# Kernel optimization log

Hardware: AMD Instinct MI355X
Metric: run time of the kernel (lower is better)

Reference implementation:

```python
import jax, jax.numpy as jnp
import numpy as np

B, C, H, W = 8, 256, 64, 64
NUM_HEADS = 4


def setup_inputs() -> dict:
    key = jax.random.key(0)
    ks = jax.random.split(key, 6)
    s = 0.02  # small init scale for 1x1 conv weights
    return {
        "x": jax.random.normal(ks[0], (B, C, H, W), jnp.float32),
        "cproj": jax.random.normal(ks[1], (B, C, H, W), jnp.float32),
        "wq": jax.random.normal(ks[2], (C, C), jnp.float32) * s,
        "bq": jnp.zeros((C,), jnp.float32),
        "wkv": jax.random.normal(ks[3], (2 * C, C), jnp.float32) * s,
        "bkv": jnp.zeros((2 * C,), jnp.float32),
        "wo": jax.random.normal(ks[4], (C, C), jnp.float32) * s,  # zero_module in torch; random here for a meaningful baseline
        "bo": jnp.zeros((C,), jnp.float32),
    }


def reference(x, cproj, wq, bq, wkv, bkv, wo, bo):
    Bb, Cc, Hh, Ww = x.shape
    N = Hh * Ww
    h = NUM_HEADS
    d = Cc // h
    scale = 1.0 / jnp.sqrt(jnp.sqrt(jnp.asarray(Cc, jnp.float32)))

    xf = x.reshape(Bb, Cc, N)
    cf = cproj.reshape(Bb, Cc, N)

    # 1x1 convs == channel matmuls
    Q = jnp.einsum('oc,bcn->bon', wq, xf) + bq[None, :, None]           # (B,C,N)
    KV = jnp.einsum('oc,bcn->bon', wkv, cf) + bkv[None, :, None]        # (B,2C,N)
    K, V = KV[:, :Cc], KV[:, Cc:]

    # softmax over channel-dim-within-head for q, over spatial N for k
    q = jax.nn.softmax(Q.reshape(Bb, h, d, N) * scale, axis=2).reshape(Bb, Cc, N)
    k = jax.nn.softmax(K.reshape(Bb, h, d, N), axis=3).reshape(Bb, Cc, N)

    # linear-attention: (B,C,C) context, then project back to N — note heads are mixed, per original bmm
    context = jnp.einsum('bcn,bdn->bcd', k, V)
    out = jnp.einsum('bcd,bdn->bcn', context, q)

    out = jnp.einsum('oc,bcn->bon', wo, out) + bo[None, :, None]
    return out.reshape(Bb, Cc, Hh, Ww)
```

## Files before the change

### kernel.cpp

```cpp
#include <hip/hip_runtime.h>

#define B_ 8
#define C_ 256
#define N_ 4096
#define NSPLIT 8

typedef float f32x4 __attribute__((ext_vector_type(4)));
typedef __bf16 bf16x8 __attribute__((ext_vector_type(8)));
typedef unsigned short u16x8 __attribute__((ext_vector_type(8)));
typedef unsigned short u16x4 __attribute__((ext_vector_type(4)));

__device__ __forceinline__ unsigned short f2bf(float f) {
  unsigned u = __float_as_uint(f);
  u += 0x7fff + ((u >> 16) & 1);
  return (unsigned short)(u >> 16);
}

__device__ __forceinline__ f32x4 mfma16(bf16x8 a, bf16x8 b, f32x4 c) {
  return __builtin_amdgcn_mfma_f32_16x16x32_bf16(a, b, c, 0, 0, 0);
}

typedef __attribute__((address_space(1))) const void* gvp;
typedef __attribute__((address_space(3))) void* lvp;
__device__ __forceinline__ void gld16(const void* g, void* l) {
  __builtin_amdgcn_global_load_lds((gvp)g, (lvp)l, 16, 0, 0);
}

template <int ROWS>
__device__ __forceinline__ void stage(unsigned short* lds, const unsigned short* g,
                                      int ld, int w, int lane) {
  const int r8 = lane >> 3;
  const int ce = ((lane & 7) ^ r8) << 3;
  const unsigned short* gp = g + (size_t)(w * (ROWS / 4) + r8) * ld + ce;
  unsigned short* lp = lds + w * (ROWS / 4) * 64;
#pragma unroll
  for (int i = 0; i < ROWS / 32; i++)
    gld16(gp + (size_t)(i * 8) * ld, lp + i * 512);
}

__device__ __forceinline__ bf16x8 frag(const unsigned short* lds, int row, int kc) {
  return *(const bf16x8*)(lds + row * 64 + ((kc ^ (row & 7)) << 3));
}

__global__ __launch_bounds__(256) void castw(
    const float* __restrict__ wq, const float* __restrict__ wkv,
    const float* __restrict__ wo, unsigned short* __restrict__ wqb,
    unsigned short* __restrict__ wkvb, unsigned short* __restrict__ wob) {
  int i = (blockIdx.x * 256 + threadIdx.x) * 4;
  const float* src;
  unsigned short* dst;
  int off;
  if (i < 65536) { src = wq; dst = wqb; off = i; }
  else if (i < 196608) { src = wkv; dst = wkvb; off = i - 65536; }
  else { src = wo; dst = wob; off = i - 196608; }
  float4 v = *(const float4*)(src + off);
  *(u16x4*)(dst + off) = (u16x4){f2bf(v.x), f2bf(v.y), f2bf(v.z), f2bf(v.w)};
}

__global__ __launch_bounds__(256) void transpose_cast(
    const float* __restrict__ x, const float* __restrict__ cp,
    unsigned short* __restrict__ xT, unsigned short* __restrict__ cpT) {
  __shared__ unsigned short tr[64][72];
  const int z = blockIdx.z, b = z >> 1;
  const float* src = (z & 1) ? cp : x;
  unsigned short* dst = (z & 1) ? cpT : xT;
  const int c0 = blockIdx.y * 64, n0 = blockIdx.x * 64;
  const int t = threadIdx.x;
  const int row = t >> 2, cg = (t & 3) * 16;
  const float* sp = src + ((size_t)b * C_ + c0 + row) * N_ + n0 + cg;
#pragma unroll
  for (int j = 0; j < 16; j += 4) {
    float4 v = *(const float4*)(sp + j);
    tr[cg + j + 0][row] = f2bf(v.x);
    tr[cg + j + 1][row] = f2bf(v.y);
    tr[cg + j + 2][row] = f2bf(v.z);
    tr[cg + j + 3][row] = f2bf(v.w);
  }
  __syncthreads();
  unsigned short* dp = dst + ((size_t)b * N_ + n0 + row) * C_ + c0 + cg;
  *(u16x8*)dp = *(const u16x8*)&tr[row][cg];
  *(u16x8*)(dp + 8) = *(const u16x8*)&tr[row][cg + 8];
}

__global__ __launch_bounds__(256) void qproj(
    const unsigned short* __restrict__ wqb, const unsigned short* __restrict__ xT,
    const float* __restrict__ bq, unsigned short* __restrict__ qT) {
  __shared__ __align__(16) unsigned short As[128 * 64];
  __shared__ __align__(16) unsigned short Bs[128 * 64];
  const int b = blockIdx.z, m0 = blockIdx.y * 128, n0 = blockIdx.x * 128;
  const int tid = threadIdx.x, lane = tid & 63, w = tid >> 6;
  const int m0w = (w >> 1) * 64, n0w = (w & 1) * 64;
  const int colL = lane & 15, kq = lane >> 4, quad = lane >> 4;
  const unsigned short* Ag = wqb + (size_t)m0 * C_;
  const unsigned short* Bg = xT + ((size_t)b * N_ + n0) * C_;

  f32x4 acc[4][4];
#pragma unroll
  for (int i = 0; i < 4; i++)
#pragma unroll
    for (int j = 0; j < 4; j++) acc[i][j] = (f32x4){0.f, 0.f, 0.f, 0.f};

  for (int kt = 0; kt < 4; kt++) {
    stage<128>(As, Ag + kt * 64, C_, w, lane);
    stage<128>(Bs, Bg + kt * 64, C_, w, lane);
    __syncthreads();
#pragma unroll
    for (int ks = 0; ks < 2; ks++) {
      bf16x8 af[4], bf[4];
#pragma unroll
      for (int mt = 0; mt < 4; mt++) af[mt] = frag(As, m0w + mt * 16 + colL, ks * 4 + kq);
#pragma unroll
      for (int nt = 0; nt < 4; nt++) bf[nt] = frag(Bs, n0w + nt * 16 + colL, ks * 4 + kq);
#pragma unroll
      for (int mt = 0; mt < 4; mt++)
#pragma unroll
        for (int nt = 0; nt < 4; nt++) acc[mt][nt] = mfma16(af[mt], bf[nt], acc[mt][nt]);
    }
    __syncthreads();
  }

#pragma unroll
  for (int nt = 0; nt < 4; nt++) {
    float v[16];
    float mx = -1e30f;
#pragma unroll
    for (int mt = 0; mt < 4; mt++)
#pragma unroll
      for (int r = 0; r < 4; r++) {
        int m = m0 + m0w + mt * 16 + quad * 4 + r;
        float val = (acc[mt][nt][r] + bq[m]) * 0.25f;
        v[mt * 4 + r] = val;
        mx = fmaxf(mx, val);
      }
    mx = fmaxf(mx, __shfl_xor(mx, 16));
    mx = fmaxf(mx, __shfl_xor(mx, 32));
    float s = 0.f;
#pragma unroll
    for (int j = 0; j < 16; j++) { v[j] = __expf(v[j] - mx); s += v[j]; }
    s += __shfl_xor(s, 16);
    s += __shfl_xor(s, 32);
    float inv = 1.0f / s;
    const int n = n0 + n0w + nt * 16 + colL;
    unsigned short* qb = qT + ((size_t)b * N_ + n) * C_ + m0 + m0w;
#pragma unroll
    for (int mt = 0; mt < 4; mt++) {
      u16x4 o = (u16x4){f2bf(v[mt * 4 + 0] * inv), f2bf(v[mt * 4 + 1] * inv),
                        f2bf(v[mt * 4 + 2] * inv), f2bf(v[mt * 4 + 3] * inv)};
      *(u16x4*)(qb + mt * 16 + quad * 4) = o;
    }
  }
}

__global__ __launch_bounds__(256) void kvproj(
    const unsigned short* __restrict__ wkvb, const unsigned short* __restrict__ cpT,
    const float* __restrict__ bkv, float* __restrict__ Kf,
    unsigned short* __restrict__ Vb) {
  __shared__ __align__(16) unsigned short As[128 * 64];
  __shared__ __align__(16) unsigned short Bs[128 * 64];
  const int b = blockIdx.z, m0 = blockIdx.y * 128, n0 = blockIdx.x * 128;
  const int tid = threadIdx.x, lane = tid & 63, w = tid >> 6;
  const int m0w = (w >> 1) * 64, n0w = (w & 1) * 64;
  const int colL = lane & 15, kq = lane >> 4, quad = lane >> 4;
  const unsigned short* Ag = wkvb + (size_t)m0 * C_;
  const unsigned short* Bg = cpT + ((size_t)b * N_ + n0) * C_;

  f32x4 acc[4][4];
#pragma unroll
  for (int i = 0; i < 4; i++)
#pragma unroll
    for (int j = 0; j < 4; j++) acc[i][j] = (f32x4){0.f, 0.f, 0.f, 0.f};

  for (int kt = 0; kt < 4; kt++) {
    stage<128>(As, Ag + kt * 64, C_, w, lane);
    stage<128>(Bs, Bg + kt * 64, C_, w, lane);
    __syncthreads();
#pragma unroll
    for (int ks = 0; ks < 2; ks++) {
      bf16x8 af[4], bf[4];
#pragma unroll
      for (int mt = 0; mt < 4; mt++) af[mt] = frag(As, m0w + mt * 16 + colL, ks * 4 + kq);
#pragma unroll
      for (int nt = 0; nt < 4; nt++) bf[nt] = frag(Bs, n0w + nt * 16 + colL, ks * 4 + kq);
#pragma unroll
      for (int mt = 0; mt < 4; mt++)
#pragma unroll
        for (int nt = 0; nt < 4; nt++) acc[mt][nt] = mfma16(af[mt], bf[nt], acc[mt][nt]);
    }
    __syncthreads();
  }

#pragma unroll
  for (int mt = 0; mt < 4; mt++)
#pragma unroll
    for (int r = 0; r < 4; r++) {
      int m = m0 + m0w + mt * 16 + quad * 4 + r;
      float bias = bkv[m];
      if (m < C_) {
        float* kr = Kf + ((size_t)b * C_ + m) * N_ + n0 + n0w;
#pragma unroll
        for (int nt = 0; nt < 4; nt++) kr[nt * 16 + colL] = acc[mt][nt][r] + bias;
      } else {
        unsigned short* vr = Vb + ((size_t)b * C_ + m - C_) * N_ + n0 + n0w;
#pragma unroll
        for (int nt = 0; nt < 4; nt++) vr[nt * 16 + colL] = f2bf(acc[mt][nt][r] + bias);
      }
    }
}

__global__ __launch_bounds__(256) void ksoftmax(const float* __restrict__ Kf,
                                                unsigned short* __restrict__ kb) {
  const int b = blockIdx.x >> 8, c = blockIdx.x & 255;
  const float* row = Kf + ((size_t)b * C_ + c) * N_;
  unsigned short* orow = kb + ((size_t)b * C_ + c) * N_;
  const int t = threadIdx.x, lane = t & 63, wv = t >> 6;
  __shared__ float red[8];

  float4 v[4];
  float mx = -1e30f;
#pragma unroll
  for (int i = 0; i < 4; i++) {
    v[i] = *(const float4*)&row[i * 1024 + t * 4];
    mx = fmaxf(fmaxf(fmaxf(mx, v[i].x), fmaxf(v[i].y, v[i].z)), v[i].w);
  }
#pragma unroll
  for (int o = 32; o > 0; o >>= 1) mx = fmaxf(mx, __shfl_down(mx, o));
  if (lane == 0) red[wv] = mx;
  __syncthreads();
  mx = fmaxf(fmaxf(red[0], red[1]), fmaxf(red[2], red[3]));

  float s = 0.f;
#pragma unroll
  for (int i = 0; i < 4; i++) {
    v[i].x = __expf(v[i].x - mx); v[i].y = __expf(v[i].y - mx);
    v[i].z = __expf(v[i].z - mx); v[i].w = __expf(v[i].w - mx);
    s += v[i].x + v[i].y + v[i].z + v[i].w;
  }
#pragma unroll
  for (int o = 32; o > 0; o >>= 1) s += __shfl_down(s, o);
  if (lane == 0) red[4 + wv] = s;
  __syncthreads();
  float inv = 1.0f / (red[4] + red[5] + red[6] + red[7]);
#pragma unroll
  for (int i = 0; i < 4; i++) {
    u16x4 o = (u16x4){f2bf(v[i].x * inv), f2bf(v[i].y * inv),
                      f2bf(v[i].z * inv), f2bf(v[i].w * inv)};
    *(u16x4*)&orow[i * 1024 + t * 4] = o;
  }
}

__global__ __launch_bounds__(256) void ctx_part(
    const unsigned short* __restrict__ kb, const unsigned short* __restrict__ Vb,
    float* __restrict__ ctxp) {
  __shared__ __align__(16) unsigned short As[128 * 64];
  __shared__ __align__(16) unsigned short Bs[64 * 64];
  const int z = blockIdx.z, b = z >> 3, s = z & 7;
  const int m0 = blockIdx.y * 128, n0 = blockIdx.x * 64;
  const int tid = threadIdx.x, lane = tid & 63, w = tid >> 6;
  const int m0w = (w & 1) * 64, n0w = (w >> 1) * 32;
  const int colL = lane & 15, kq = lane >> 4, quad = lane >> 4;
  const unsigned short* Ag = kb + ((size_t)b * C_ + m0) * N_;
  const unsigned short* Bg = Vb + ((size_t)b * C_ + n0) * N_;
  const int kbeg = s * (N_ / NSPLIT);

  f32x4 acc[4][2];
#pragma unroll
  for (int i = 0; i < 4; i++)
#pragma unroll
    for (int j = 0; j < 2; j++) acc[i][j] = (f32x4){0.f, 0.f, 0.f, 0.f};

  for (int kt = 0; kt < (N_ / NSPLIT) / 64; kt++) {
    stage<128>(As, Ag + kbeg + kt * 64, N_, w, lane);
    stage<64>(Bs, Bg + kbeg + kt * 64, N_, w, lane);
    __syncthreads();
#pragma unroll
    for (int ks = 0; ks < 2; ks++) {
      bf16x8 af[4], bf[2];
#pragma unroll
      for (int mt = 0; mt < 4; mt++) af[mt] = frag(As, m0w + mt * 16 + colL, ks * 4 + kq);
#pragma unroll
      for (int nt = 0; nt < 2; nt++) bf[nt] = frag(Bs, n0w + nt * 16 + colL, ks * 4 + kq);
#pragma unroll
      for (int mt = 0; mt < 4; mt++)
#pragma unroll
        for (int nt = 0; nt < 2; nt++) acc[mt][nt] = mfma16(af[mt], bf[nt], acc[mt][nt]);
    }
    __syncthreads();
  }

  float* outp = ctxp + ((size_t)s * B_ + b) * C_ * C_;
#pragma unroll
  for (int mt = 0; mt < 4; mt++)
#pragma unroll
    for (int nt = 0; nt < 2; nt++)
#pragma unroll
      for (int r = 0; r < 4; r++) {
        int m = m0 + m0w + mt * 16 + quad * 4 + r;
        int n = n0 + n0w + nt * 16 + colL;
        outp[(size_t)m * C_ + n] = acc[mt][nt][r];
      }
}

__global__ __launch_bounds__(256) void ctx_reduce_t(const float* __restrict__ ctxp,
                                                    unsigned short* __restrict__ ctxsT) {
  __shared__ unsigned short t[64][72];
  const int b = blockIdx.z, c0 = blockIdx.y * 64, d0 = blockIdx.x * 64;
  const int tid = threadIdx.x;
  const int cl = tid >> 2, dg = (tid & 3) * 16;
  const float* base = ctxp + ((size_t)b * C_ + c0 + cl) * C_ + d0 + dg;
  float acc[16];
#pragma unroll
  for (int j = 0; j < 16; j++) acc[j] = 0.f;
  for (int s = 0; s < NSPLIT; s++) {
    const float* p = base + (size_t)s * B_ * C_ * C_;
#pragma unroll
    for (int j = 0; j < 16; j += 4) {
      float4 v = *(const float4*)(p + j);
      acc[j] += v.x; acc[j + 1] += v.y; acc[j + 2] += v.z; acc[j + 3] += v.w;
    }
  }
#pragma unroll
  for (int j = 0; j < 16; j++) t[dg + j][cl] = f2bf(acc[j]);
  __syncthreads();
  const int dr = tid >> 2, cg = (tid & 3) * 16;
  unsigned short* dp = ctxsT + ((size_t)b * C_ + d0 + dr) * C_ + c0 + cg;
  *(u16x8*)dp = *(const u16x8*)&t[dr][cg];
  *(u16x8*)(dp + 8) = *(const u16x8*)&t[dr][cg + 8];
}

__global__ __launch_bounds__(256) void oproj(
    const unsigned short* __restrict__ wob, const unsigned short* __restrict__ ctxsT,
    unsigned short* __restrict__ ctx2) {
  __shared__ __align__(16) unsigned short As[128 * 64];
  __shared__ __align__(16) unsigned short Bs[128 * 64];
  const int b = blockIdx.z, m0 = blockIdx.y * 128, n0 = blockIdx.x * 128;
  const int tid = threadIdx.x, lane = tid & 63, w = tid >> 6;
  const int m0w = (w >> 1) * 64, n0w = (w & 1) * 64;
  const int colL = lane & 15, kq = lane >> 4, quad = lane >> 4;
  const unsigned short* Ag = wob + (size_t)m0 * C_;
  const unsigned short* Bg = ctxsT + ((size_t)b * C_ + n0) * C_;

  f32x4 acc[4][4];
#pragma unroll
  for (int i = 0; i < 4; i++)
#pragma unroll
    for (int j = 0; j < 4; j++) acc[i][j] = (f32x4){0.f, 0.f, 0.f, 0.f};

  for (int kt = 0; kt < 4; kt++) {
    stage<128>(As, Ag + kt * 64, C_, w, lane);
    stage<128>(Bs, Bg + kt * 64, C_, w, lane);
    __syncthreads();
#pragma unroll
    for (int ks = 0; ks < 2; ks++) {
      bf16x8 af[4], bf[4];
#pragma unroll
      for (int mt = 0; mt < 4; mt++) af[mt] = frag(As, m0w + mt * 16 + colL, ks * 4 + kq);
#pragma unroll
      for (int nt = 0; nt < 4; nt++) bf[nt] = frag(Bs, n0w + nt * 16 + colL, ks * 4 + kq);
#pragma unroll
      for (int mt = 0; mt < 4; mt++)
#pragma unroll
        for (int nt = 0; nt < 4; nt++) acc[mt][nt] = mfma16(af[mt], bf[nt], acc[mt][nt]);
    }
    __syncthreads();
  }

  unsigned short* ob = ctx2 + (size_t)b * C_ * C_;
#pragma unroll
  for (int mt = 0; mt < 4; mt++)
#pragma unroll
    for (int nt = 0; nt < 4; nt++)
#pragma unroll
      for (int r = 0; r < 4; r++) {
        int m = m0 + m0w + mt * 16 + quad * 4 + r;
        int n = n0 + n0w + nt * 16 + colL;
        ob[(size_t)m * C_ + n] = f2bf(acc[mt][nt][r]);
      }
}

__global__ __launch_bounds__(256) void outgemm(
    const unsigned short* __restrict__ ctx2, const unsigned short* __restrict__ qT,
    const float* __restrict__ bo, float* __restrict__ out) {
  __shared__ __align__(16) unsigned short As[128 * 64];
  __shared__ __align__(16) unsigned short Bs[128 * 64];
  const int b = blockIdx.z, n0 = blockIdx.x * 128, m0 = blockIdx.y * 128;
  const int tid = threadIdx.x, lane = tid & 63, w = tid >> 6;
  const int m0w = (w >> 1) * 64, n0w = (w & 1) * 64;
  const int colL = lane & 15, kq = lane >> 4, quad = lane >> 4;
  const unsigned short* Ag = ctx2 + ((size_t)b * C_ + m0) * C_;
  const unsigned short* Bg = qT + ((size_t)b * N_ + n0) * C_;

  f32x4 acc[4][4];
#pragma unroll
  for (int i = 0; i < 4; i++)
#pragma unroll
    for (int j = 0; j < 4; j++) acc[i][j] = (f32x4){0.f, 0.f, 0.f, 0.f};

  for (int kt = 0; kt < 4; kt++) {
    stage<128>(As, Ag + kt * 64, C_, w, lane);
    stage<128>(Bs, Bg + kt * 64, C_, w, lane);
    __syncthreads();
#pragma unroll
    for (int ks = 0; ks < 2; ks++) {
      bf16x8 af[4], bf[4];
#pragma unroll
      for (int mt = 0; mt < 4; mt++) af[mt] = frag(As, m0w + mt * 16 + colL, ks * 4 + kq);
#pragma unroll
      for (int nt = 0; nt < 4; nt++) bf[nt] = frag(Bs, n0w + nt * 16 + colL, ks * 4 + kq);
#pragma unroll
      for (int mt = 0; mt < 4; mt++)
#pragma unroll
        for (int nt = 0; nt < 4; nt++) acc[mt][nt] = mfma16(af[mt], bf[nt], acc[mt][nt]);
    }
    __syncthreads();
  }

  float* ob = out + (size_t)b * C_ * N_;
#pragma unroll
  for (int mt = 0; mt < 4; mt++)
#pragma unroll
    for (int r = 0; r < 4; r++) {
      int m = m0 + m0w + mt * 16 + quad * 4 + r;
      float bias = bo[m];
#pragma unroll
      for (int nt = 0; nt < 4; nt++) {
        int n = n0 + n0w + nt * 16 + colL;
        ob[(size_t)m * N_ + n] = acc[mt][nt][r] + bias;
      }
    }
}

extern "C" void kernel_launch(void* const* d_in, const int* in_sizes, int n_in,
                              void* d_out, int out_size, void* d_ws, size_t ws_size,
                              hipStream_t stream) {
  const float* x     = (const float*)d_in[0];
  const float* cproj = (const float*)d_in[1];
  const float* wq    = (const float*)d_in[2];
  const float* bq    = (const float*)d_in[3];
  const float* wkv   = (const float*)d_in[4];
  const float* bkv   = (const float*)d_in[5];
  const float* wo    = (const float*)d_in[6];
  const float* bo    = (const float*)d_in[7];
  float* out = (float*)d_out;

  unsigned short* xT    = (unsigned short*)d_ws;
  unsigned short* cpT   = xT + 8388608;
  unsigned short* qT    = cpT + 8388608;
  float*          Kf    = (float*)(qT + 8388608);
  unsigned short* Vb    = (unsigned short*)(Kf + 8388608);
  unsigned short* wqb   = Vb + 8388608;
  unsigned short* wkvb  = wqb + 65536;
  unsigned short* wob   = wkvb + 131072;
  unsigned short* ctxsT = wob + 65536;
  unsigned short* ctx2  = ctxsT + 524288;
  unsigned short* kb    = xT;
  float*          ctxp  = (float*)cpT;

  castw<<<256, 256, 0, stream>>>(wq, wkv, wo, wqb, wkvb, wob);
  transpose_cast<<<dim3(64, 4, 16), 256, 0, stream>>>(x, cproj, xT, cpT);
  qproj<<<dim3(32, 2, 8), 256, 0, stream>>>(wqb, xT, bq, qT);
  kvproj<<<dim3(32, 4, 8), 256, 0, stream>>>(wkvb, cpT, bkv, Kf, Vb);
  ksoftmax<<<2048, 256, 0, stream>>>(Kf, kb);
  ctx_part<<<dim3(4, 2, 64), 256, 0, stream>>>(kb, Vb, ctxp);
  ctx_reduce_t<<<dim3(4, 4, 8), 256, 0, stream>>>(ctxp, ctxsT);
  oproj<<<dim3(2, 2, 8), 256, 0, stream>>>(wob, ctxsT, ctx2);
  outgemm<<<dim3(32, 2, 8), 256, 0, stream>>>(ctx2, qT, bo, out);
}
```

Baseline: 205.2 us.

## Retile projection GEMMs to full-M tiles and coalesce transpose_cast loads

The Q, KV and output GEMMs now each use one block covering all output channels over a 64-column N tile. Each activation tile is staged once instead of being reloaded by several M-blocks, and each wave owns a 64- or 128-row slab. The transpose_cast kernel now reads four rows per thread with float4 loads and writes packed u16x4 into shared memory, replacing the scalar LDS stores. The cost is more LDS per block (up to 72 KB for kvproj), more accumulator registers in kvproj (32 tiles per wave), and restaging the whole weight matrix in every block, all of which may lower occupancy.

```diff
diff --git a/kernel.cpp b/kernel.cpp
--- a/kernel.cpp
+++ b/kernel.cpp
@@ -66,32 +66,34 @@
   unsigned short* dst = (z & 1) ? cpT : xT;
   const int c0 = blockIdx.y * 64, n0 = blockIdx.x * 64;
   const int t = threadIdx.x;
-  const int row = t >> 2, cg = (t & 3) * 16;
-  const float* sp = src + ((size_t)b * C_ + c0 + row) * N_ + n0 + cg;
-#pragma unroll
-  for (int j = 0; j < 16; j += 4) {
-    float4 v = *(const float4*)(sp + j);
-    tr[cg + j + 0][row] = f2bf(v.x);
-    tr[cg + j + 1][row] = f2bf(v.y);
-    tr[cg + j + 2][row] = f2bf(v.z);
-    tr[cg + j + 3][row] = f2bf(v.w);
+  const int r0 = (t >> 4) * 4;
+  const int nq = (t & 15) * 4;
+  const float* sp = src + ((size_t)b * C_ + c0 + r0) * N_ + n0 + nq;
+  float4 v[4];
+#pragma unroll
+  for (int i = 0; i < 4; i++) v[i] = *(const float4*)(sp + (size_t)i * N_);
+#pragma unroll
+  for (int j = 0; j < 4; j++) {
+    u16x4 o = (u16x4){f2bf(((const float*)&v[0])[j]), f2bf(((const float*)&v[1])[j]),
+                      f2bf(((const float*)&v[2])[j]), f2bf(((const float*)&v[3])[j])};
+    *(u16x4*)&tr[nq + j][r0] = o;
   }
   __syncthreads();
-  unsigned short* dp = dst + ((size_t)b * N_ + n0 + row) * C_ + c0 + cg;
-  *(u16x8*)dp = *(const u16x8*)&tr[row][cg];
-  *(u16x8*)(dp + 8) = *(const u16x8*)&tr[row][cg + 8];
+  const int nr = t >> 2, cg = (t & 3) * 16;
+  unsigned short* dp = dst + ((size_t)b * N_ + n0 + nr) * C_ + c0 + cg;
+  *(u16x8*)dp = *(const u16x8*)&tr[nr][cg];
+  *(u16x8*)(dp + 8) = *(const u16x8*)&tr[nr][cg + 8];
 }
 
 __global__ __launch_bounds__(256) void qproj(
     const unsigned short* __restrict__ wqb, const unsigned short* __restrict__ xT,
     const float* __restrict__ bq, unsigned short* __restrict__ qT) {
-  __shared__ __align__(16) unsigned short As[128 * 64];
-  __shared__ __align__(16) unsigned short Bs[128 * 64];
-  const int b = blockIdx.z, m0 = blockIdx.y * 128, n0 = blockIdx.x * 128;
+  __shared__ __align__(16) unsigned short As[256 * 64];
+  __shared__ __align__(16) unsigned short Bs[64 * 64];
+  const int b = blockIdx.z, n0 = blockIdx.x * 64;
   const int tid = threadIdx.x, lane = tid & 63, w = tid >> 6;
-  const int m0w = (w >> 1) * 64, n0w = (w & 1) * 64;
+  const int m0w = w * 64;
   const int colL = lane & 15, kq = lane >> 4, quad = lane >> 4;
-  const unsigned short* Ag = wqb + (size_t)m0 * C_;
   const unsigned short* Bg = xT + ((size_t)b * N_ + n0) * C_;
 
   f32x4 acc[4][4];
@@ -101,8 +103,8 @@
     for (int j = 0; j < 4; j++) acc[i][j] = (f32x4){0.f, 0.f, 0.f, 0.f};
 
   for (int kt = 0; kt < 4; kt++) {
-    stage<128>(As, Ag + kt * 64, C_, w, lane);
-    stage<128>(Bs, Bg + kt * 64, C_, w, lane);
+    stage<256>(As, wqb + kt * 64, C_, w, lane);
+    stage<64>(Bs, Bg + kt * 64, C_, w, lane);
     __syncthreads();
 #pragma unroll
     for (int ks = 0; ks < 2; ks++) {
@@ -110,7 +112,7 @@
 #pragma unroll
       for (int mt = 0; mt < 4; mt++) af[mt] = frag(As, m0w + mt * 16 + colL, ks * 4 + kq);
 #pragma unroll
-      for (int nt = 0; nt < 4; nt++) bf[nt] = frag(Bs, n0w + nt * 16 + colL, ks * 4 + kq);
+      for (int nt = 0; nt < 4; nt++) bf[nt] = frag(Bs, nt * 16 + colL, ks * 4 + kq);
 #pragma unroll
       for (int mt = 0; mt < 4; mt++)
 #pragma unroll
@@ -127,7 +129,7 @@
     for (int mt = 0; mt < 4; mt++)
 #pragma unroll
       for (int r = 0; r < 4; r++) {
-        int m = m0 + m0w + mt * 16 + quad * 4 + r;
+        int m = m0w + mt * 16 + quad * 4 + r;
         float val = (acc[mt][nt][r] + bq[m]) * 0.25f;
         v[mt * 4 + r] = val;
         mx = fmaxf(mx, val);
@@ -140,8 +142,8 @@
     s += __shfl_xor(s, 16);
     s += __shfl_xor(s, 32);
     float inv = 1.0f / s;
-    const int n = n0 + n0w + nt * 16 + colL;
-    unsigned short* qb = qT + ((size_t)b * N_ + n) * C_ + m0 + m0w;
+    const int n = n0 + nt * 16 + colL;
+    unsigned short* qb = qT + ((size_t)b * N_ + n) * C_ + m0w;
 #pragma unroll
     for (int mt = 0; mt < 4; mt++) {
       u16x4 o = (u16x4){f2bf(v[mt * 4 + 0] * inv), f2bf(v[mt * 4 + 1] * inv),
@@ -155,52 +157,51 @@
     const unsigned short* __restrict__ wkvb, const unsigned short* __restrict__ cpT,
     const float* __restrict__ bkv, float* __restrict__ Kf,
     unsigned short* __restrict__ Vb) {
-  __shared__ __align__(16) unsigned short As[128 * 64];
-  __shared__ __align__(16) unsigned short Bs[128 * 64];
-  const int b = blockIdx.z, m0 = blockIdx.y * 128, n0 = blockIdx.x * 128;
+  __shared__ __align__(16) unsigned short As[512 * 64];
+  __shared__ __align__(16) unsigned short Bs[64 * 64];
+  const int b = blockIdx.z, n0 = blockIdx.x * 64;
   const int tid = threadIdx.x, lane = tid & 63, w = tid >> 6;
-  const int m0w = (w >> 1) * 64, n0w = (w & 1) * 64;
+  const int m0w = w * 128;
   const int colL = lane & 15, kq = lane >> 4, quad = lane >> 4;
-  const unsigned short* Ag = wkvb + (size_t)m0 * C_;
   const unsigned short* Bg = cpT + ((size_t)b * N_ + n0) * C_;
 
-  f32x4 acc[4][4];
-#pragma unroll
-  for (int i = 0; i < 4; i++)
+  f32x4 acc[8][4];
+#pragma unroll
+  for (int i = 0; i < 8; i++)
 #pragma unroll
     for (int j = 0; j < 4; j++) acc[i][j] = (f32x4){0.f, 0.f, 0.f, 0.f};
 
   for (int kt = 0; kt < 4; kt++) {
-    stage<128>(As, Ag + kt * 64, C_, w, lane);
-    stage<128>(Bs, Bg + kt * 64, C_, w, lane);
+    stage<512>(As, wkvb + kt * 64, C_, w, lane);
+    stage<64>(Bs, Bg + kt * 64, C_, w, lane);
     __syncthreads();
 #pragma unroll
     for (int ks = 0; ks < 2; ks++) {
-      bf16x8 af[4], bf[4];
-#pragma unroll
-      for (int mt = 0; mt < 4; mt++) af[mt] = frag(As, m0w + mt * 16 + colL, ks * 4 + kq);
-#pragma unroll
-      for (int nt = 0; nt < 4; nt++) bf[nt] = frag(Bs, n0w + nt * 16 + colL, ks * 4 + kq);
-#pragma unroll
-      for (int mt = 0; mt < 4; mt++)
-#pragma unroll
-        for (int nt = 0; nt < 4; nt++) acc[mt][nt] = mfma16(af[mt], bf[nt], acc[mt][nt]);
-    }
-    __syncthreads();
-  }
-
-#pragma unroll
-  for (int mt = 0; mt < 4; mt++)
+      bf16x8 bf[4];
+#pragma unroll
+      for (int nt = 0; nt < 4; nt++) bf[nt] = frag(Bs, nt * 16 + colL, ks * 4 + kq);
+#pragma unroll
+      for (int mt = 0; mt < 8; mt++) {
+        bf16x8 af = frag(As, m0w + mt * 16 + colL, ks * 4 + kq);
+#pragma unroll
+        for (int nt = 0; nt < 4; nt++) acc[mt][nt] = mfma16(af, bf[nt], acc[mt][nt]);
+      }
+    }
+    __syncthreads();
+  }
+
+#pragma unroll
+  for (int mt = 0; mt < 8; mt++)
 #pragma unroll
     for (int r = 0; r < 4; r++) {
-      int m = m0 + m0w + mt * 16 + quad * 4 + r;
+      int m = m0w + mt * 16 + quad * 4 + r;
       float bias = bkv[m];
       if (m < C_) {
-        float* kr = Kf + ((size_t)b * C_ + m) * N_ + n0 + n0w;
+        float* kr = Kf + ((size_t)b * C_ + m) * N_ + n0;
 #pragma unroll
         for (int nt = 0; nt < 4; nt++) kr[nt * 16 + colL] = acc[mt][nt][r] + bias;
       } else {
-        unsigned short* vr = Vb + ((size_t)b * C_ + m - C_) * N_ + n0 + n0w;
+        unsigned short* vr = Vb + ((size_t)b * C_ + m - C_) * N_ + n0;
 #pragma unroll
         for (int nt = 0; nt < 4; nt++) vr[nt * 16 + colL] = f2bf(acc[mt][nt][r] + bias);
       }
@@ -380,13 +381,13 @@
 __global__ __launch_bounds__(256) void outgemm(
     const unsigned short* __restrict__ ctx2, const unsigned short* __restrict__ qT,
     const float* __restrict__ bo, float* __restrict__ out) {
-  __shared__ __align__(16) unsigned short As[128 * 64];
-  __shared__ __align__(16) unsigned short Bs[128 * 64];
-  const int b = blockIdx.z, n0 = blockIdx.x * 128, m0 = blockIdx.y * 128;
+  __shared__ __align__(16) unsigned short As[256 * 64];
+  __shared__ __align__(16) unsigned short Bs[64 * 64];
+  const int b = blockIdx.z, n0 = blockIdx.x * 64;
   const int tid = threadIdx.x, lane = tid & 63, w = tid >> 6;
-  const int m0w = (w >> 1) * 64, n0w = (w & 1) * 64;
+  const int m0w = w * 64;
   const int colL = lane & 15, kq = lane >> 4, quad = lane >> 4;
-  const unsigned short* Ag = ctx2 + ((size_t)b * C_ + m0) * C_;
+  const unsigned short* Ag = ctx2 + (size_t)b * C_ * C_;
   const unsigned short* Bg = qT + ((size_t)b * N_ + n0) * C_;
 
   f32x4 acc[4][4];
@@ -396,8 +397,8 @@
     for (int j = 0; j < 4; j++) acc[i][j] = (f32x4){0.f, 0.f, 0.f, 0.f};
 
   for (int kt = 0; kt < 4; kt++) {
-    stage<128>(As, Ag + kt * 64, C_, w, lane);
-    stage<128>(Bs, Bg + kt * 64, C_, w, lane);
+    stage<256>(As, Ag + kt * 64, C_, w, lane);
+    stage<64>(Bs, Bg + kt * 64, C_, w, lane);
     __syncthreads();
 #pragma unroll
     for (int ks = 0; ks < 2; ks++) {
@@ -405,7 +406,7 @@
 #pragma unroll
       for (int mt = 0; mt < 4; mt++) af[mt] = frag(As, m0w + mt * 16 + colL, ks * 4 + kq);
 #pragma unroll
-      for (int nt = 0; nt < 4; nt++) bf[nt] = frag(Bs, n0w + nt * 16 + colL, ks * 4 + kq);
+      for (int nt = 0; nt < 4; nt++) bf[nt] = frag(Bs, nt * 16 + colL, ks * 4 + kq);
 #pragma unroll
       for (int mt = 0; mt < 4; mt++)
 #pragma unroll
@@ -419,11 +420,11 @@
   for (int mt = 0; mt < 4; mt++)
 #pragma unroll
     for (int r = 0; r < 4; r++) {
-      int m = m0 + m0w + mt * 16 + quad * 4 + r;
+      int m = m0w + mt * 16 + quad * 4 + r;
       float bias = bo[m];
 #pragma unroll
       for (int nt = 0; nt < 4; nt++) {
-        int n = n0 + n0w + nt * 16 + colL;
+        int n = n0 + nt * 16 + colL;
         ob[(size_t)m * N_ + n] = acc[mt][nt][r] + bias;
       }
     }
@@ -457,11 +458,11 @@
 
   castw<<<256, 256, 0, stream>>>(wq, wkv, wo, wqb, wkvb, wob);
   transpose_cast<<<dim3(64, 4, 16), 256, 0, stream>>>(x, cproj, xT, cpT);
-  qproj<<<dim3(32, 2, 8), 256, 0, stream>>>(wqb, xT, bq, qT);
-  kvproj<<<dim3(32, 4, 8), 256, 0, stream>>>(wkvb, cpT, bkv, Kf, Vb);
+  qproj<<<dim3(64, 1, 8), 256, 0, stream>>>(wqb, xT, bq, qT);
+  kvproj<<<dim3(64, 1, 8), 256, 0, stream>>>(wkvb, cpT, bkv, Kf, Vb);
   ksoftmax<<<2048, 256, 0, stream>>>(Kf, kb);
   ctx_part<<<dim3(4, 2, 64), 256, 0, stream>>>(kb, Vb, ctxp);
   ctx_reduce_t<<<dim3(4, 4, 8), 256, 0, stream>>>(ctxp, ctxsT);
   oproj<<<dim3(2, 2, 8), 256, 0, stream>>>(wob, ctxsT, ctx2);
-  outgemm<<<dim3(32, 2, 8), 256, 0, stream>>>(ctx2, qT, bo, out);
-}
+  outgemm<<<dim3(64, 1, 8), 256, 0, stream>>>(ctx2, qT, bo, out);
+}
```

Measured after the change: 213.5 us. 4.1% more time.
